# Optimization experiments

Hardware: AMD Instinct MI355X
Metric: run time of the kernel (lower is better)

Reference implementation:

```python
import jax, jax.numpy as jnp
import numpy as np

B, S, H, DH, W, G, M = 2, 4096, 12, 64, 256, 64, 256
D = H * DH  # 768
VOCAB = 50282
NEG = -1e9


def setup_inputs() -> dict:
    key = jax.random.key(0)
    ks = jax.random.split(key, 16)
    f = lambda k, shp, s=0.02: jax.random.normal(k, shp, jnp.float32) * s
    return {
        'input_ids': jax.random.randint(ks[0], (B, S), 0, VOCAB, jnp.int32),
        'attn_mask': jnp.ones((B, S), jnp.float32),
        'html_idx': jnp.sort(jax.random.randint(ks[1], (B, M), 0, S, jnp.int32), axis=-1),
        'embed': f(ks[2], (VOCAB, D), 1.0),
        'Wq': f(ks[3], (D, D)), 'bq': jnp.zeros((D,), jnp.float32),
        'Wk': f(ks[4], (D, D)), 'bk': jnp.zeros((D,), jnp.float32),
        'Wv': f(ks[5], (D, D)), 'bv': jnp.zeros((D,), jnp.float32),
        'Wo': f(ks[6], (D, D)), 'bo': jnp.zeros((D,), jnp.float32),
        'gamma': jnp.ones((D,), jnp.float32), 'beta': jnp.zeros((D,), jnp.float32),
        'Wp': f(ks[7], (D, D)), 'bp': jnp.zeros((D,), jnp.float32),
        'Wa': f(ks[8], (D, 3)), 'ba': jnp.zeros((3,), jnp.float32),
        'Ws': f(ks[9], (D, 2)), 'bs': jnp.zeros((2,), jnp.float32),
    }


def _band_shift(t, n_chunks):
    # t: [..., n_chunks+2, W, ...chunked along axis -3/-2]; gather 3 neighbor chunks
    return jnp.concatenate([t[..., i:i + n_chunks, :, :] for i in range(3)], axis=-2)


def longformer_hpt(input_ids, attn_mask, html_idx, embed, Wq, bq, Wk, bk, Wv, bv,
                   Wo, bo, gamma, beta, Wp, bp, Wa, ba, Ws, bs):
    x = embed[input_ids]  # [B,S,D]
    heads = lambda t: t.reshape(B, S, H, DH).transpose(0, 2, 1, 3)  # [B,H,S,DH]
    q, k, v = heads(x @ Wq + bq), heads(x @ Wk + bk), heads(x @ Wv + bv)
    scale = 1.0 / np.sqrt(DH).astype(np.float32)
    C = S // W  # chunks

    # --- sliding-window (banded) attention, one-sided window W ---
    kp = jnp.pad(k, ((0, 0), (0, 0), (W, W), (0, 0))).reshape(B, H, C + 2, W, DH)
    vp = jnp.pad(v, ((0, 0), (0, 0), (W, W), (0, 0))).reshape(B, H, C + 2, W, DH)
    k3 = _band_shift(kp, C)  # [B,H,C,3W,DH]
    v3 = _band_shift(vp, C)
    qc = q.reshape(B, H, C, W, DH)
    sb = jnp.einsum('bhcqd,bhckd->bhcqk', qc, k3) * scale  # [B,H,C,W,3W]

    ii = jnp.arange(W)[:, None]
    jj = jnp.arange(3 * W)[None, :]
    band_ok = jnp.abs(jj - W - ii) <= W  # [W,3W]
    keypos = jnp.arange(C)[:, None] * W - W + jnp.arange(3 * W)[None, :]  # [C,3W]
    kvalid = (keypos >= 0) & (keypos < S) & (keypos >= G)  # global keys handled separately
    mp = jnp.pad(attn_mask, ((0, 0), (W, W))).reshape(B, C + 2, W)
    m3 = jnp.concatenate([mp[:, i:i + C] for i in range(3)], axis=2)  # [B,C,3W]
    mask = band_ok[None, :, :] & kvalid[:, None, :] & (m3[:, :, None, :] > 0)[..., :, :].reshape(B, C, 1, 3 * W).astype(bool) if False else (band_ok[None, None, :, :] & kvalid[None, :, None, :] & (m3[:, :, None, :] > 0))  # [B,C,W,3W]
    sb = jnp.where(mask[:, None], sb, NEG).reshape(B, H, S, 3 * W)

    # --- all tokens also attend to the G global tokens ---
    kg, vg = k[:, :, :G], v[:, :, :G]
    sg = jnp.einsum('bhsd,bhgd->bhsg', q, kg) * scale
    sg = jnp.where(attn_mask[:, None, None, :G] > 0, sg, NEG)

    p = jax.nn.softmax(jnp.concatenate([sg, sb], -1), -1)  # [B,H,S,G+3W]
    pg, pb = p[..., :G], p[..., G:].reshape(B, H, C, W, 3 * W)
    out = (jnp.einsum('bhcqk,bhckd->bhcqd', pb, v3).reshape(B, H, S, DH)
           + jnp.einsum('bhsg,bhgd->bhsd', pg, vg))

    # --- global queries attend to everything ---
    sgl = jnp.einsum('bhgd,bhsd->bhgs', q[:, :, :G], k) * scale
    sgl = jnp.where(attn_mask[:, None, None, :] > 0, sgl, NEG)
    outg = jnp.einsum('bhgs,bhsd->bhgd', jax.nn.softmax(sgl, -1), v)
    out = jnp.concatenate([outg, out[:, :, G:]], axis=2)

    ctx = out.transpose(0, 2, 1, 3).reshape(B, S, D)
    h = x + ctx @ Wo + bo
    mu = h.mean(-1, keepdims=True)
    var = ((h - mu) ** 2).mean(-1, keepdims=True)
    hn = (h - mu) / jnp.sqrt(var + 1e-5) * gamma + beta  # last_hidden [B,S,D]

    # probes (ans_probe: Linear(768,3)+Sigmoid, span_probe: Linear(768,2)+Sigmoid)
    ans = jax.nn.sigmoid(hn @ Wa + ba)
    span = jax.nn.sigmoid(hn @ Ws + bs)

    # ReIndexer gather of HTML-element hidden states + ConditionCalculator
    hr = jnp.take_along_axis(hn, html_idx[:, :, None].astype(jnp.int32), axis=1)  # [B,M,D]
    t = jax.nn.relu(hr @ Wp + bp)
    cond = jax.nn.sigmoid(jnp.einsum('bqh,bch->bcq', hr, t))  # [B,M,M]
    return hn, ans, span, cond


def reference(input_ids, attn_mask, html_idx, embed, Wq, bq, Wk, bk, Wv, bv,
              Wo, bo, gamma, beta, Wp, bp, Wa, ba, Ws, bs):
    return longformer_hpt(input_ids, attn_mask, html_idx, embed, Wq, bq, Wk, bk,
                          Wv, bv, Wo, bo, gamma, beta, Wp, bp, Wa, ba, Ws, bs)
```

## Files before the change

### kernel.cpp

```cpp
#include <hip/hip_runtime.h>

typedef unsigned short u16;
typedef unsigned int   u32;
typedef __attribute__((ext_vector_type(8))) short s8v;
typedef __attribute__((ext_vector_type(8))) unsigned short us8;
typedef __attribute__((ext_vector_type(4))) float f4v;

constexpr int BC  = 2;
constexpr int SL  = 4096;
constexpr int NH  = 12;
constexpr int HD  = 64;
constexpr int DM  = 768;
constexpr int WIN = 256;
constexpr int GLB = 64;
constexpr int QN  = 2304;
constexpr int KCH = 16;
constexpr float FOLD = 0.125f * 1.44269504088896f;
constexpr float NEGS = -1.0e9f;

__device__ __forceinline__ float b2f(u16 b){ return __uint_as_float(((u32)b) << 16); }
__device__ __forceinline__ u16 f2b(float f){
  u32 u = __float_as_uint(f);
  return (u16)((u + 0x7fffu + ((u >> 16) & 1u)) >> 16);
}
__device__ __forceinline__ float wredsum(float v){
  #pragma unroll
  for (int o = 32; o > 0; o >>= 1) v += __shfl_xor(v, o, 64);
  return v;
}
__device__ __forceinline__ float sigf(float x){ return 1.f / (1.f + __expf(-x)); }

__global__ void transpose_pack(const float* __restrict__ src, u16* __restrict__ dst, int N){
  int e = blockIdx.x*256 + threadIdx.x;
  if (e >= N*768) return;
  int n = e / 768, k = e - n*768;
  dst[e] = f2b(src[(long)k*N + n]);
}

__global__ void pack_bias(const float* __restrict__ bq, const float* __restrict__ bk,
                          const float* __restrict__ bv, float* __restrict__ dst){
  int i = blockIdx.x*256 + threadIdx.x;
  if (i >= 2304) return;
  dst[i] = (i < 768) ? bq[i] : (i < 1536) ? bk[i-768] : bv[i-1536];
}

__global__ void embed_gather(const int* __restrict__ ids, const float* __restrict__ emb,
                             float* __restrict__ x, u16* __restrict__ xb){
  int e4 = blockIdx.x*256 + threadIdx.x;
  if (e4 >= 8192*192) return;
  int row = e4 / 192, d4 = e4 - row*192;
  int id = ids[row];
  float4 v = ((const float4*)(emb + (long)id*768))[d4];
  ((float4*)(x + (long)row*768))[d4] = v;
  u32 p0 = (u32)f2b(v.x) | ((u32)f2b(v.y) << 16);
  u32 p1 = (u32)f2b(v.z) | ((u32)f2b(v.w) << 16);
  ((u32*)(xb + (long)row*768))[d4*2]   = p0;
  ((u32*)(xb + (long)row*768))[d4*2+1] = p1;
}

__global__ void gather_hr(const int* __restrict__ hidx, const float* __restrict__ hn,
                          u16* __restrict__ hrb){
  int e = blockIdx.x*256 + threadIdx.x;
  if (e >= 512*768) return;
  int r = e / 768, d = e - r*768;
  int b = r >> 8;
  int idx = hidx[r];
  hrb[e] = f2b(hn[((long)(b*SL + idx))*768 + d]);
}

template<int MODE>
__global__ __launch_bounds__(256, 2)
void gemm_bt(const u16* __restrict__ A, const u16* __restrict__ Bt,
             const float* __restrict__ bias, const float* __restrict__ res,
             float* __restrict__ outF, u16* __restrict__ outB,
             int M, int N, int K, long sA, long sB, long sO)
{
  const int bz = blockIdx.z;
  A  += (long)bz * sA;
  Bt += (long)bz * sB;
  const int n0 = blockIdx.x * 128;
  const int m0 = blockIdx.y * 128;
  __shared__ u16 lsA[128*64];
  __shared__ u16 lsB[128*64];
  const int t = threadIdx.x;
  const int w = t >> 6, lane = t & 63;
  const int wr = w >> 1, wc = w & 1;
  const int fr = lane & 15, fq = lane >> 4;

  f4v acc[4][4];
  #pragma unroll
  for (int i=0;i<4;i++)
    #pragma unroll
    for (int j=0;j<4;j++) acc[i][j] = (f4v)0.f;

  for (int k0 = 0; k0 < K; k0 += 64){
    #pragma unroll
    for (int i=0;i<4;i++){
      int e = (w*4+i)*512 + lane*8;
      int row = e >> 6, col = e & 63;
      __builtin_amdgcn_global_load_lds(
        (const __attribute__((address_space(1))) void*)(A + (long)(m0+row)*K + (k0+col)),
        (__attribute__((address_space(3))) void*)(&lsA[(w*4+i)*512]), 16, 0, 0);
      __builtin_amdgcn_global_load_lds(
        (const __attribute__((address_space(1))) void*)(Bt + (long)(n0+row)*K + (k0+col)),
        (__attribute__((address_space(3))) void*)(&lsB[(w*4+i)*512]), 16, 0, 0);
    }
    __syncthreads();
    #pragma unroll
    for (int kk = 0; kk < 2; kk++){
      s8v af[4], bfv[4];
      #pragma unroll
      for (int mi=0;mi<4;mi++)
        af[mi] = *(const s8v*)&lsA[(wr*64 + mi*16 + fr)*64 + kk*32 + fq*8];
      #pragma unroll
      for (int ni=0;ni<4;ni++)
        bfv[ni] = *(const s8v*)&lsB[(wc*64 + ni*16 + fr)*64 + kk*32 + fq*8];
      #pragma unroll
      for (int mi=0;mi<4;mi++)
        #pragma unroll
        for (int ni=0;ni<4;ni++)
          acc[mi][ni] = __builtin_amdgcn_mfma_f32_16x16x32_bf16(af[mi], bfv[ni], acc[mi][ni], 0, 0, 0);
    }
    __syncthreads();
  }
  #pragma unroll
  for (int mi=0;mi<4;mi++){
    #pragma unroll
    for (int ni=0;ni<4;ni++){
      #pragma unroll
      for (int r=0;r<4;r++){
        int row = m0 + wr*64 + mi*16 + fq*4 + r;
        int col = n0 + wc*64 + ni*16 + fr;
        float v = acc[mi][ni][r];
        if constexpr (MODE == 0){
          v += bias[col];
          outB[(long)row*N + col] = f2b(v);
        } else if constexpr (MODE == 1){
          v += bias[col] + res[(long)row*N + col];
          outF[(long)row*N + col] = v;
        } else if constexpr (MODE == 2){
          v = fmaxf(v + bias[col], 0.f);
          outB[(long)row*N + col] = f2b(v);
        } else {
          (outF + bz*sO)[(long)row*N + col] = sigf(v);
        }
      }
    }
  }
}

__global__ __launch_bounds__(256, 2)
void attn_band_mfma(const u16* __restrict__ qkv, const float* __restrict__ mask, u16* __restrict__ ctx)
{
  const int q0 = blockIdx.x * 64;
  const int h = blockIdx.y, b = blockIdx.z;
  const int t = threadIdx.x;
  const int w = t >> 6, lane = t & 63;
  const int fq = lane >> 4, fr = lane & 15;

  __shared__ u16 lsK[64*64];
  __shared__ u16 lsVT[64*72];
  __shared__ u16 lsP[4][16*72];
  __shared__ float lsM[64];

  const long bq = (long)b*SL*QN;
  const u16* qrow = qkv + (bq + (long)(q0 + w*16 + fr)*QN) + h*HD;
  s8v aq[2];
  aq[0] = *(const s8v*)(qrow + fq*8);
  aq[1] = *(const s8v*)(qrow + 32 + fq*8);

  const u16* kq = qkv + bq + DM + h*HD;
  const u16* vq = qkv + bq + 2*DM + h*HD;
  const float* mrow = mask + b*SL;

  f4v out[4];
  #pragma unroll
  for (int n=0;n<4;n++) out[n] = (f4v)0.f;
  float m[4]  = {-3.0e38f,-3.0e38f,-3.0e38f,-3.0e38f};
  float l[4]  = {0.f,0.f,0.f,0.f};

  for (int ti = -1; ti < 9; ++ti){
    const int k0 = (ti < 0) ? 0 : (q0 - 256 + ti*64);
    if (ti >= 0 && (k0 < GLB || k0 >= SL)) continue;
    __syncthreads();
    if (t < 64) lsM[t] = mrow[k0 + t];
    #pragma unroll
    for (int j=0;j<2;j++){
      const int r = (w*2+j)*8 + (lane>>3);
      const int d = ((lane&7) ^ (lane>>3))*8;
      __builtin_amdgcn_global_load_lds(
        (const __attribute__((address_space(1))) void*)(kq + (long)(k0+r)*QN + d),
        (__attribute__((address_space(3))) void*)(&lsK[(w*2+j)*512]), 16, 0, 0);
    }
    #pragma unroll
    for (int j=0;j<2;j++){
      const int d0 = w*8 + j*32;
      us8 vv = *(const us8*)(vq + (long)(k0+lane)*QN + d0);
      #pragma unroll
      for (int jj=0;jj<8;jj++) lsVT[(d0+jj)*72 + lane] = (u16)vv[jj];
    }
    __syncthreads();

    f4v s[4];
    #pragma unroll
    for (int n=0;n<4;n++) s[n] = (f4v)0.f;
    #pragma unroll
    for (int kk=0;kk<2;kk++){
      #pragma unroll
      for (int n=0;n<4;n++){
        s8v bf = *(const s8v*)&lsK[(16*n+fr)*64 + (((kk*4+fq) ^ (fr&7))<<3)];
        s[n] = __builtin_amdgcn_mfma_f32_16x16x32_bf16(aq[kk], bf, s[n], 0,0,0);
      }
    }
    const bool isg = (ti < 0);
    #pragma unroll
    for (int n=0;n<4;n++){
      const int kcol = 16*n + fr;
      const float mk = lsM[kcol];
      #pragma unroll
      for (int r=0;r<4;r++){
        const int dd = k0 + kcol - (q0 + w*16 + fq*4 + r);
        const bool valid = (mk > 0.f) && (isg || (dd >= -WIN && dd <= WIN));
        s[n][r] = valid ? s[n][r]*FOLD : NEGS;
      }
    }
    float sf[4];
    #pragma unroll
    for (int r=0;r<4;r++){
      float rm = fmaxf(fmaxf(s[0][r], s[1][r]), fmaxf(s[2][r], s[3][r]));
      rm = fmaxf(rm, __shfl_xor(rm, 1, 64));
      rm = fmaxf(rm, __shfl_xor(rm, 2, 64));
      rm = fmaxf(rm, __shfl_xor(rm, 4, 64));
      rm = fmaxf(rm, __shfl_xor(rm, 8, 64));
      const float mn = fmaxf(m[r], rm);
      sf[r] = exp2f(m[r] - mn);
      m[r] = mn;
    }
    u16* lsPw = lsP[w];
    float rs[4] = {0.f,0.f,0.f,0.f};
    #pragma unroll
    for (int n=0;n<4;n++){
      #pragma unroll
      for (int r=0;r<4;r++){
        float p = exp2f(s[n][r] - m[r]);
        rs[r] += p;
        lsPw[(fq*4+r)*72 + 16*n + fr] = f2b(p);
        out[n][r] *= sf[r];
      }
    }
    #pragma unroll
    for (int r=0;r<4;r++){
      float rv = rs[r];
      rv += __shfl_xor(rv, 1, 64);
      rv += __shfl_xor(rv, 2, 64);
      rv += __shfl_xor(rv, 4, 64);
      rv += __shfl_xor(rv, 8, 64);
      l[r] = l[r]*sf[r] + rv;
    }
    s8v ap[2];
    ap[0] = *(const s8v*)&lsPw[fr*72 + fq*8];
    ap[1] = *(const s8v*)&lsPw[fr*72 + 32 + fq*8];
    #pragma unroll
    for (int kk=0;kk<2;kk++){
      #pragma unroll
      for (int n=0;n<4;n++){
        s8v bv = *(const s8v*)&lsVT[(16*n+fr)*72 + kk*32 + fq*8];
        out[n] = __builtin_amdgcn_mfma_f32_16x16x32_bf16(ap[kk], bv, out[n], 0,0,0);
      }
    }
  }
  #pragma unroll
  for (int r=0;r<4;r++) l[r] = 1.f/l[r];
  u16* cb = ctx + (((long)(b*SL) + q0 + w*16 + fq*4))*DM + h*HD + fr;
  #pragma unroll
  for (int n=0;n<4;n++)
    #pragma unroll
    for (int r=0;r<4;r++)
      cb[(long)r*DM + 16*n] = f2b(out[n][r]*l[r]);
}

__global__ __launch_bounds__(256, 2)
void attn_global_part(const u16* __restrict__ qkv, const float* __restrict__ mask,
                      float* __restrict__ pout, float* __restrict__ pml)
{
  const int ck = blockIdx.x;
  const int h = blockIdx.y, b = blockIdx.z;
  const int bh = b*NH + h;
  const int t = threadIdx.x;
  const int w = t >> 6, lane = t & 63;
  const int fq = lane >> 4, fr = lane & 15;

  __shared__ u16 lsK[64*64];
  __shared__ u16 lsVT[64*72];
  __shared__ u16 lsP[4][16*72];
  __shared__ float lsM[64];

  const long bq = (long)b*SL*QN;
  const u16* qrow = qkv + (bq + (long)(w*16 + fr)*QN) + h*HD;
  s8v aq[2];
  aq[0] = *(const s8v*)(qrow + fq*8);
  aq[1] = *(const s8v*)(qrow + 32 + fq*8);

  const u16* kq = qkv + bq + DM + h*HD;
  const u16* vq = qkv + bq + 2*DM + h*HD;
  const float* mrow = mask + b*SL;

  f4v out[4];
  #pragma unroll
  for (int n=0;n<4;n++) out[n] = (f4v)0.f;
  float m[4]  = {-3.0e38f,-3.0e38f,-3.0e38f,-3.0e38f};
  float l[4]  = {0.f,0.f,0.f,0.f};

  for (int ti = 0; ti < 4; ++ti){
    const int k0 = ck*256 + ti*64;
    __syncthreads();
    if (t < 64) lsM[t] = mrow[k0 + t];
    #pragma unroll
    for (int j=0;j<2;j++){
      const int r = (w*2+j)*8 + (lane>>3);
      const int d = ((lane&7) ^ (lane>>3))*8;
      __builtin_amdgcn_global_load_lds(
        (const __attribute__((address_space(1))) void*)(kq + (long)(k0+r)*QN + d),
        (__attribute__((address_space(3))) void*)(&lsK[(w*2+j)*512]), 16, 0, 0);
    }
    #pragma unroll
    for (int j=0;j<2;j++){
      const int d0 = w*8 + j*32;
      us8 vv = *(const us8*)(vq + (long)(k0+lane)*QN + d0);
      #pragma unroll
      for (int jj=0;jj<8;jj++) lsVT[(d0+jj)*72 + lane] = (u16)vv[jj];
    }
    __syncthreads();

    f4v s[4];
    #pragma unroll
    for (int n=0;n<4;n++) s[n] = (f4v)0.f;
    #pragma unroll
    for (int kk=0;kk<2;kk++){
      #pragma unroll
      for (int n=0;n<4;n++){
        s8v bf = *(const s8v*)&lsK[(16*n+fr)*64 + (((kk*4+fq) ^ (fr&7))<<3)];
        s[n] = __builtin_amdgcn_mfma_f32_16x16x32_bf16(aq[kk], bf, s[n], 0,0,0);
      }
    }
    #pragma unroll
    for (int n=0;n<4;n++){
      const float mk = lsM[16*n + fr];
      #pragma unroll
      for (int r=0;r<4;r++)
        s[n][r] = (mk > 0.f) ? s[n][r]*FOLD : NEGS;
    }
    float sf[4];
    #pragma unroll
    for (int r=0;r<4;r++){
      float rm = fmaxf(fmaxf(s[0][r], s[1][r]), fmaxf(s[2][r], s[3][r]));
      rm = fmaxf(rm, __shfl_xor(rm, 1, 64));
      rm = fmaxf(rm, __shfl_xor(rm, 2, 64));
      rm = fmaxf(rm, __shfl_xor(rm, 4, 64));
      rm = fmaxf(rm, __shfl_xor(rm, 8, 64));
      const float mn = fmaxf(m[r], rm);
      sf[r] = exp2f(m[r] - mn);
      m[r] = mn;
    }
    u16* lsPw = lsP[w];
    float rs[4] = {0.f,0.f,0.f,0.f};
    #pragma unroll
    for (int n=0;n<4;n++){
      #pragma unroll
      for (int r=0;r<4;r++){
        float p = exp2f(s[n][r] - m[r]);
        rs[r] += p;
        lsPw[(fq*4+r)*72 + 16*n + fr] = f2b(p);
        out[n][r] *= sf[r];
      }
    }
    #pragma unroll
    for (int r=0;r<4;r++){
      float rv = rs[r];
      rv += __shfl_xor(rv, 1, 64);
      rv += __shfl_xor(rv, 2, 64);
      rv += __shfl_xor(rv, 4, 64);
      rv += __shfl_xor(rv, 8, 64);
      l[r] = l[r]*sf[r] + rv;
    }
    s8v ap[2];
    ap[0] = *(const s8v*)&lsPw[fr*72 + fq*8];
    ap[1] = *(const s8v*)&lsPw[fr*72 + 32 + fq*8];
    #pragma unroll
    for (int kk=0;kk<2;kk++){
      #pragma unroll
      for (int n=0;n<4;n++){
        s8v bv = *(const s8v*)&lsVT[(16*n+fr)*72 + kk*32 + fq*8];
        out[n] = __builtin_amdgcn_mfma_f32_16x16x32_bf16(ap[kk], bv, out[n], 0,0,0);
      }
    }
  }
  float* pob = pout + ((long)(ck*BC*NH + bh))*64*64;
  #pragma unroll
  for (int n=0;n<4;n++)
    #pragma unroll
    for (int r=0;r<4;r++)
      pob[(w*16 + fq*4 + r)*64 + 16*n + fr] = out[n][r];
  if (fr == 0){
    float* pmb = pml + ((long)(ck*BC*NH + bh))*128;
    #pragma unroll
    for (int r=0;r<4;r++){
      pmb[(w*16 + fq*4 + r)*2 + 0] = m[r];
      pmb[(w*16 + fq*4 + r)*2 + 1] = l[r];
    }
  }
}

__global__ __launch_bounds__(256, 2)
void attn_global_combine(const float* __restrict__ pout, const float* __restrict__ pml,
                         u16* __restrict__ ctx)
{
  const int bh = blockIdx.x;
  const int b = bh / NH, h = bh % NH;
  const int t = threadIdx.x;
  __shared__ float wgt[KCH][64];
  __shared__ float rl[64];
  if (t < 64){
    float mc[KCH], lc[KCH];
    #pragma unroll
    for (int c = 0; c < KCH; c++){
      const float* pmb = pml + ((long)(c*BC*NH + bh))*128 + t*2;
      mc[c] = pmb[0]; lc[c] = pmb[1];
    }
    float M = mc[0];
    #pragma unroll
    for (int c = 1; c < KCH; c++) M = fmaxf(M, mc[c]);
    float L = 0.f;
    #pragma unroll
    for (int c = 0; c < KCH; c++){
      const float wv = exp2f(mc[c] - M);
      wgt[c][t] = wv;
      L += lc[c]*wv;
    }
    rl[t] = 1.f/L;
  }
  __syncthreads();
  const int row = t >> 2, dseg = t & 3;
  float acc[16];
  #pragma unroll
  for (int i=0;i<16;i++) acc[i] = 0.f;
  for (int c = 0; c < KCH; c++){
    const float wv = wgt[c][row];
    const float4* pb = (const float4*)(pout + ((long)(c*BC*NH + bh)*64 + row)*64 + dseg*16);
    #pragma unroll
    for (int i = 0; i < 4; i++){
      float4 v = pb[i];
      acc[i*4+0] += v.x*wv; acc[i*4+1] += v.y*wv;
      acc[i*4+2] += v.z*wv; acc[i*4+3] += v.w*wv;
    }
  }
  u16* cr = ctx + ((long)(b*SL + row))*DM + h*HD + dseg*16;
  const float r = rl[row];
  #pragma unroll
  for (int i = 0; i < 16; i += 2){
    u32 pk = (u32)f2b(acc[i]*r) | ((u32)f2b(acc[i+1]*r) << 16);
    *(u32*)(cr + i) = pk;
  }
}

__global__ __launch_bounds__(256, 2)
void ln_heads(const float* __restrict__ hbuf, const float* __restrict__ gamma, const float* __restrict__ beta,
              const float* __restrict__ Wa, const float* __restrict__ ba,
              const float* __restrict__ Wsp, const float* __restrict__ bsp,
              float* __restrict__ hn, float* __restrict__ ans, float* __restrict__ span)
{
  const int r = blockIdx.x;
  const int t = threadIdx.x, lane = t & 63, w = t >> 6;
  __shared__ float red[8];
  __shared__ float dred[4][5];
  const float* hrow = hbuf + (long)r*DM;
  float v0 = hrow[t], v1 = hrow[t+256], v2 = hrow[t+512];
  float sum = wredsum(v0 + v1 + v2);
  float sq  = wredsum(v0*v0 + v1*v1 + v2*v2);
  if (lane == 0){ red[w] = sum; red[4+w] = sq; }
  __syncthreads();
  const float mu  = (red[0]+red[1]+red[2]+red[3]) * (1.f/768.f);
  const float msq = (red[4]+red[5]+red[6]+red[7]) * (1.f/768.f);
  const float rstd = rsqrtf(msq - mu*mu + 1e-5f);
  float pa0=0,pa1=0,pa2=0,ps0=0,ps1=0;
  const long base = (long)r*DM;
  #pragma unroll
  for (int jj = 0; jj < 3; jj++){
    const int i = t + jj*256;
    const float hv = (jj==0) ? v0 : (jj==1) ? v1 : v2;
    const float y = (hv - mu)*rstd*gamma[i] + beta[i];
    hn[base + i] = y;
    pa0 += y*Wa[i*3+0]; pa1 += y*Wa[i*3+1]; pa2 += y*Wa[i*3+2];
    ps0 += y*Wsp[i*2+0]; ps1 += y*Wsp[i*2+1];
  }
  pa0 = wredsum(pa0); pa1 = wredsum(pa1); pa2 = wredsum(pa2);
  ps0 = wredsum(ps0); ps1 = wredsum(ps1);
  if (lane == 0){ dred[w][0]=pa0; dred[w][1]=pa1; dred[w][2]=pa2; dred[w][3]=ps0; dred[w][4]=ps1; }
  __syncthreads();
  if (t == 0){
    float A0 = dred[0][0]+dred[1][0]+dred[2][0]+dred[3][0];
    float A1 = dred[0][1]+dred[1][1]+dred[2][1]+dred[3][1];
    float A2 = dred[0][2]+dred[1][2]+dred[2][2]+dred[3][2];
    float S0 = dred[0][3]+dred[1][3]+dred[2][3]+dred[3][3];
    float S1 = dred[0][4]+dred[1][4]+dred[2][4]+dred[3][4];
    ans[(long)r*3+0]  = sigf(A0 + ba[0]);
    ans[(long)r*3+1]  = sigf(A1 + ba[1]);
    ans[(long)r*3+2]  = sigf(A2 + ba[2]);
    span[(long)r*2+0] = sigf(S0 + bsp[0]);
    span[(long)r*2+1] = sigf(S1 + bsp[1]);
  }
}

extern "C" void kernel_launch(void* const* d_in, const int* in_sizes, int n_in,
                              void* d_out, int out_size, void* d_ws, size_t ws_size,
                              hipStream_t stream)
{
  const int*   input_ids = (const int*)  d_in[0];
  const float* attn_mask = (const float*)d_in[1];
  const int*   html_idx  = (const int*)  d_in[2];
  const float* embed     = (const float*)d_in[3];
  const float* Wq = (const float*)d_in[4];  const float* bq = (const float*)d_in[5];
  const float* Wk = (const float*)d_in[6];  const float* bk = (const float*)d_in[7];
  const float* Wv = (const float*)d_in[8];  const float* bv = (const float*)d_in[9];
  const float* Wo = (const float*)d_in[10]; const float* bo = (const float*)d_in[11];
  const float* gamma = (const float*)d_in[12]; const float* beta = (const float*)d_in[13];
  const float* Wp = (const float*)d_in[14]; const float* bp = (const float*)d_in[15];
  const float* Wa = (const float*)d_in[16]; const float* ba = (const float*)d_in[17];
  const float* Wsp = (const float*)d_in[18]; const float* bsp = (const float*)d_in[19];

  char* ws = (char*)d_ws;
  size_t off = 0;
  auto take = [&](size_t bytes)->char*{
    char* p = ws + off; off += (bytes + 255) & ~(size_t)255; return p;
  };
  float* x_f    = (float*)take((size_t)8192*768*4);
  u16*   x_b    = (u16*)  take((size_t)8192*768*2);
  u16*   wt_qkv = (u16*)  take((size_t)2304*768*2);
  u16*   wt_o   = (u16*)  take((size_t)768*768*2);
  u16*   wt_p   = (u16*)  take((size_t)768*768*2);
  float* b_qkv  = (float*)take(2304*4);
  u16*   qkv_b  = (u16*)  take((size_t)8192*2304*2);
  u16*   ctx_b  = (u16*)  take((size_t)8192*768*2);
  float* h_f    = (float*)take((size_t)8192*768*4);
  u16*   hr_b   = (u16*)  take((size_t)512*768*2);
  u16*   t_b    = (u16*)  take((size_t)512*768*2);
  float* pout   = (float*)take((size_t)KCH*BC*NH*64*64*4);
  float* pml    = (float*)take((size_t)KCH*BC*NH*128*4);

  float* out_hn   = (float*)d_out;
  float* out_ans  = out_hn  + (size_t)8192*768;
  float* out_span = out_ans + (size_t)8192*3;
  float* out_cond = out_span + (size_t)8192*2;

  transpose_pack<<<2304, 256, 0, stream>>>(Wq, wt_qkv,             768);
  transpose_pack<<<2304, 256, 0, stream>>>(Wk, wt_qkv +   768*768, 768);
  transpose_pack<<<2304, 256, 0, stream>>>(Wv, wt_qkv + 2*768*768, 768);
  transpose_pack<<<2304, 256, 0, stream>>>(Wo, wt_o, 768);
  transpose_pack<<<2304, 256, 0, stream>>>(Wp, wt_p, 768);
  pack_bias<<<9, 256, 0, stream>>>(bq, bk, bv, b_qkv);
  embed_gather<<<6144, 256, 0, stream>>>(input_ids, embed, x_f, x_b);

  gemm_bt<0><<<dim3(18,64,1), 256, 0, stream>>>(x_b, wt_qkv, b_qkv, nullptr,
                                                nullptr, qkv_b, 8192, 2304, 768, 0,0,0);
  attn_band_mfma<<<dim3(64,12,2), 256, 0, stream>>>(qkv_b, attn_mask, ctx_b);
  attn_global_part<<<dim3(KCH,12,2), 256, 0, stream>>>(qkv_b, attn_mask, pout, pml);
  attn_global_combine<<<BC*NH, 256, 0, stream>>>(pout, pml, ctx_b);
  gemm_bt<1><<<dim3(6,64,1), 256, 0, stream>>>(ctx_b, wt_o, bo, x_f,
                                               h_f, nullptr, 8192, 768, 768, 0,0,0);
  ln_heads<<<8192, 256, 0, stream>>>(h_f, gamma, beta, Wa, ba, Wsp, bsp,
                                     out_hn, out_ans, out_span);
  gather_hr<<<1536, 256, 0, stream>>>(html_idx, out_hn, hr_b);
  gemm_bt<2><<<dim3(6,4,1), 256, 0, stream>>>(hr_b, wt_p, bp, nullptr,
                                              nullptr, t_b, 512, 768, 768, 0,0,0);
  gemm_bt<3><<<dim3(2,2,2), 256, 0, stream>>>(t_b, hr_b, nullptr, nullptr,
                                              out_cond, nullptr, 256, 256, 768,
                                              (long)256*768, (long)256*768, (long)256*256);
}
```

Measured before the change: 263.3 us.

## Double-buffer attention tiles, fuse weight packing, drop fp32 residual copy

Five per-matrix transpose launches and the bias pack are merged into one LDS-tiled transpose kernel with coalesced reads and writes. Both attention kernels now double-buffer K/V/mask tiles, prefetching the next tile while computing the current one. The band kernel computes its valid tile range up front instead of skipping tiles inside the loop, and occupancy hints rise to 3 blocks per SIMD. The fp32 embedding copy is removed and the residual is read from the bf16 copy, saving memory traffic but adding bf16 rounding to the residual path.

```diff
diff --git a/kernel.cpp b/kernel.cpp
--- a/kernel.cpp
+++ b/kernel.cpp
@@ -30,28 +30,49 @@
 }
 __device__ __forceinline__ float sigf(float x){ return 1.f / (1.f + __expf(-x)); }
 
-__global__ void transpose_pack(const float* __restrict__ src, u16* __restrict__ dst, int N){
-  int e = blockIdx.x*256 + threadIdx.x;
-  if (e >= N*768) return;
-  int n = e / 768, k = e - n*768;
-  dst[e] = f2b(src[(long)k*N + n]);
-}
-
-__global__ void pack_bias(const float* __restrict__ bq, const float* __restrict__ bk,
-                          const float* __restrict__ bv, float* __restrict__ dst){
-  int i = blockIdx.x*256 + threadIdx.x;
-  if (i >= 2304) return;
-  dst[i] = (i < 768) ? bq[i] : (i < 1536) ? bk[i-768] : bv[i-1536];
+__global__ void pack_w(const float* __restrict__ Wq, const float* __restrict__ Wk,
+                       const float* __restrict__ Wv, const float* __restrict__ Wo,
+                       const float* __restrict__ Wp,
+                       const float* __restrict__ bq, const float* __restrict__ bk,
+                       const float* __restrict__ bv,
+                       u16* __restrict__ wt_qkv, u16* __restrict__ wt_o,
+                       u16* __restrict__ wt_p, float* __restrict__ b_qkv)
+{
+  __shared__ float tile[64][65];
+  const int bid = blockIdx.x;
+  const int mi = bid / 144, rest = bid % 144;
+  const int kt = rest / 12, ntc = rest % 12;
+  const float* src = (mi==0)?Wq:(mi==1)?Wk:(mi==2)?Wv:(mi==3)?Wo:Wp;
+  u16* dst = (mi<3) ? (wt_qkv + (size_t)mi*768*768) : ((mi==3) ? wt_o : wt_p);
+  const int t = threadIdx.x;
+  const int k0 = kt*64, n0 = ntc*64;
+  #pragma unroll
+  for (int i=0;i<4;i++){
+    const int r = (t>>4) + i*16;
+    float4 v = ((const float4*)(src + (long)(k0+r)*768 + n0))[t&15];
+    tile[r][(t&15)*4+0] = v.x; tile[r][(t&15)*4+1] = v.y;
+    tile[r][(t&15)*4+2] = v.z; tile[r][(t&15)*4+3] = v.w;
+  }
+  __syncthreads();
+  const int n = t & 63, kc = (t>>6)*16;
+  u32* d32 = (u32*)(dst + (long)(n0+n)*768 + k0 + kc);
+  #pragma unroll
+  for (int i=0;i<8;i++){
+    d32[i] = (u32)f2b(tile[kc+2*i][n]) | ((u32)f2b(tile[kc+2*i+1][n]) << 16);
+  }
+  if (bid < 9){
+    const int i = bid*256 + t;
+    if (i < 2304) b_qkv[i] = (i < 768) ? bq[i] : (i < 1536) ? bk[i-768] : bv[i-1536];
+  }
 }
 
 __global__ void embed_gather(const int* __restrict__ ids, const float* __restrict__ emb,
-                             float* __restrict__ x, u16* __restrict__ xb){
+                             u16* __restrict__ xb){
   int e4 = blockIdx.x*256 + threadIdx.x;
   if (e4 >= 8192*192) return;
   int row = e4 / 192, d4 = e4 - row*192;
   int id = ids[row];
   float4 v = ((const float4*)(emb + (long)id*768))[d4];
-  ((float4*)(x + (long)row*768))[d4] = v;
   u32 p0 = (u32)f2b(v.x) | ((u32)f2b(v.y) << 16);
   u32 p1 = (u32)f2b(v.z) | ((u32)f2b(v.w) << 16);
   ((u32*)(xb + (long)row*768))[d4*2]   = p0;
@@ -71,7 +92,7 @@
 template<int MODE>
 __global__ __launch_bounds__(256, 2)
 void gemm_bt(const u16* __restrict__ A, const u16* __restrict__ Bt,
-             const float* __restrict__ bias, const float* __restrict__ res,
+             const float* __restrict__ bias, const u16* __restrict__ resB,
              float* __restrict__ outF, u16* __restrict__ outB,
              int M, int N, int K, long sA, long sB, long sO)
 {
@@ -136,7 +157,7 @@
           v += bias[col];
           outB[(long)row*N + col] = f2b(v);
         } else if constexpr (MODE == 1){
-          v += bias[col] + res[(long)row*N + col];
+          v += bias[col] + b2f(resB[(long)row*N + col]);
           outF[(long)row*N + col] = v;
         } else if constexpr (MODE == 2){
           v = fmaxf(v + bias[col], 0.f);
@@ -149,7 +170,7 @@
   }
 }
 
-__global__ __launch_bounds__(256, 2)
+__global__ __launch_bounds__(256, 3)
 void attn_band_mfma(const u16* __restrict__ qkv, const float* __restrict__ mask, u16* __restrict__ ctx)
 {
   const int q0 = blockIdx.x * 64;
@@ -158,10 +179,10 @@
   const int w = t >> 6, lane = t & 63;
   const int fq = lane >> 4, fr = lane & 15;
 
-  __shared__ u16 lsK[64*64];
-  __shared__ u16 lsVT[64*72];
+  __shared__ u16 lsK[2][64*64];
+  __shared__ u16 lsVT[2][64*72];
   __shared__ u16 lsP[4][16*72];
-  __shared__ float lsM[64];
+  __shared__ float lsM[2][64];
 
   const long bq = (long)b*SL*QN;
   const u16* qrow = qkv + (bq + (long)(q0 + w*16 + fr)*QN) + h*HD;
@@ -173,33 +194,45 @@
   const u16* vq = qkv + bq + 2*DM + h*HD;
   const float* mrow = mask + b*SL;
 
+  const int ti_lo = (q0 < 320) ? ((320 - q0) >> 6) : 0;
+  const int ti_hi_raw = (4352 - q0) >> 6;
+  const int ti_hi = ti_hi_raw < 9 ? ti_hi_raw : 9;
+  const int NTT = 1 + (ti_hi - ti_lo);
+  const int kb0 = q0 - 256 + ti_lo*64;
+
   f4v out[4];
   #pragma unroll
   for (int n=0;n<4;n++) out[n] = (f4v)0.f;
   float m[4]  = {-3.0e38f,-3.0e38f,-3.0e38f,-3.0e38f};
   float l[4]  = {0.f,0.f,0.f,0.f};
 
-  for (int ti = -1; ti < 9; ++ti){
-    const int k0 = (ti < 0) ? 0 : (q0 - 256 + ti*64);
-    if (ti >= 0 && (k0 < GLB || k0 >= SL)) continue;
-    __syncthreads();
-    if (t < 64) lsM[t] = mrow[k0 + t];
+  us8 vv0, vv1;
+  auto stage_issue = [&](int i, int buf){
+    const int k0 = (i == 0) ? 0 : kb0 + (i-1)*64;
+    if (t < 64) lsM[buf][t] = mrow[k0 + t];
     #pragma unroll
     for (int j=0;j<2;j++){
       const int r = (w*2+j)*8 + (lane>>3);
       const int d = ((lane&7) ^ (lane>>3))*8;
       __builtin_amdgcn_global_load_lds(
         (const __attribute__((address_space(1))) void*)(kq + (long)(k0+r)*QN + d),
-        (__attribute__((address_space(3))) void*)(&lsK[(w*2+j)*512]), 16, 0, 0);
-    }
-    #pragma unroll
-    for (int j=0;j<2;j++){
-      const int d0 = w*8 + j*32;
-      us8 vv = *(const us8*)(vq + (long)(k0+lane)*QN + d0);
-      #pragma unroll
-      for (int jj=0;jj<8;jj++) lsVT[(d0+jj)*72 + lane] = (u16)vv[jj];
-    }
+        (__attribute__((address_space(3))) void*)(&lsK[buf][(w*2+j)*512]), 16, 0, 0);
+    }
+    vv0 = *(const us8*)(vq + (long)(k0+lane)*QN + w*8);
+    vv1 = *(const us8*)(vq + (long)(k0+lane)*QN + w*8 + 32);
+  };
+
+  stage_issue(0, 0);
+  int cur = 0;
+  for (int i = 0; i < NTT; i++){
+    const int k0 = (i == 0) ? 0 : kb0 + (i-1)*64;
+    const int d0 = w*8;
+    #pragma unroll
+    for (int jj=0;jj<8;jj++) lsVT[cur][(d0+jj)*72 + lane] = (u16)vv0[jj];
+    #pragma unroll
+    for (int jj=0;jj<8;jj++) lsVT[cur][(d0+32+jj)*72 + lane] = (u16)vv1[jj];
     __syncthreads();
+    if (i+1 < NTT) stage_issue(i+1, cur^1);
 
     f4v s[4];
     #pragma unroll
@@ -208,15 +241,15 @@
     for (int kk=0;kk<2;kk++){
       #pragma unroll
       for (int n=0;n<4;n++){
-        s8v bf = *(const s8v*)&lsK[(16*n+fr)*64 + (((kk*4+fq) ^ (fr&7))<<3)];
+        s8v bf = *(const s8v*)&lsK[cur][(16*n+fr)*64 + (((kk*4+fq) ^ (fr&7))<<3)];
         s[n] = __builtin_amdgcn_mfma_f32_16x16x32_bf16(aq[kk], bf, s[n], 0,0,0);
       }
     }
-    const bool isg = (ti < 0);
+    const bool isg = (i == 0);
     #pragma unroll
     for (int n=0;n<4;n++){
       const int kcol = 16*n + fr;
-      const float mk = lsM[kcol];
+      const float mk = lsM[cur][kcol];
       #pragma unroll
       for (int r=0;r<4;r++){
         const int dd = k0 + kcol - (q0 + w*16 + fq*4 + r);
@@ -264,10 +297,11 @@
     for (int kk=0;kk<2;kk++){
       #pragma unroll
       for (int n=0;n<4;n++){
-        s8v bv = *(const s8v*)&lsVT[(16*n+fr)*72 + kk*32 + fq*8];
+        s8v bv = *(const s8v*)&lsVT[cur][(16*n+fr)*72 + kk*32 + fq*8];
         out[n] = __builtin_amdgcn_mfma_f32_16x16x32_bf16(ap[kk], bv, out[n], 0,0,0);
       }
     }
+    cur ^= 1;
   }
   #pragma unroll
   for (int r=0;r<4;r++) l[r] = 1.f/l[r];
@@ -279,7 +313,7 @@
       cb[(long)r*DM + 16*n] = f2b(out[n][r]*l[r]);
 }
 
-__global__ __launch_bounds__(256, 2)
+__global__ __launch_bounds__(256, 3)
 void attn_global_part(const u16* __restrict__ qkv, const float* __restrict__ mask,
                       float* __restrict__ pout, float* __restrict__ pml)
 {
@@ -290,10 +324,10 @@
   const int w = t >> 6, lane = t & 63;
   const int fq = lane >> 4, fr = lane & 15;
 
-  __shared__ u16 lsK[64*64];
-  __shared__ u16 lsVT[64*72];
+  __shared__ u16 lsK[2][64*64];
+  __shared__ u16 lsVT[2][64*72];
   __shared__ u16 lsP[4][16*72];
-  __shared__ float lsM[64];
+  __shared__ float lsM[2][64];
 
   const long bq = (long)b*SL*QN;
   const u16* qrow = qkv + (bq + (long)(w*16 + fr)*QN) + h*HD;
@@ -311,26 +345,32 @@
   float m[4]  = {-3.0e38f,-3.0e38f,-3.0e38f,-3.0e38f};
   float l[4]  = {0.f,0.f,0.f,0.f};
 
-  for (int ti = 0; ti < 4; ++ti){
-    const int k0 = ck*256 + ti*64;
-    __syncthreads();
-    if (t < 64) lsM[t] = mrow[k0 + t];
+  us8 vv0, vv1;
+  auto stage_issue = [&](int i, int buf){
+    const int k0 = ck*256 + i*64;
+    if (t < 64) lsM[buf][t] = mrow[k0 + t];
     #pragma unroll
     for (int j=0;j<2;j++){
       const int r = (w*2+j)*8 + (lane>>3);
       const int d = ((lane&7) ^ (lane>>3))*8;
       __builtin_amdgcn_global_load_lds(
         (const __attribute__((address_space(1))) void*)(kq + (long)(k0+r)*QN + d),
-        (__attribute__((address_space(3))) void*)(&lsK[(w*2+j)*512]), 16, 0, 0);
-    }
-    #pragma unroll
-    for (int j=0;j<2;j++){
-      const int d0 = w*8 + j*32;
-      us8 vv = *(const us8*)(vq + (long)(k0+lane)*QN + d0);
-      #pragma unroll
-      for (int jj=0;jj<8;jj++) lsVT[(d0+jj)*72 + lane] = (u16)vv[jj];
-    }
+        (__attribute__((address_space(3))) void*)(&lsK[buf][(w*2+j)*512]), 16, 0, 0);
+    }
+    vv0 = *(const us8*)(vq + (long)(k0+lane)*QN + w*8);
+    vv1 = *(const us8*)(vq + (long)(k0+lane)*QN + w*8 + 32);
+  };
+
+  stage_issue(0, 0);
+  int cur = 0;
+  for (int i = 0; i < 4; i++){
+    const int d0 = w*8;
+    #pragma unroll
+    for (int jj=0;jj<8;jj++) lsVT[cur][(d0+jj)*72 + lane] = (u16)vv0[jj];
+    #pragma unroll
+    for (int jj=0;jj<8;jj++) lsVT[cur][(d0+32+jj)*72 + lane] = (u16)vv1[jj];
     __syncthreads();
+    if (i+1 < 4) stage_issue(i+1, cur^1);
 
     f4v s[4];
     #pragma unroll
@@ -339,13 +379,13 @@
     for (int kk=0;kk<2;kk++){
       #pragma unroll
       for (int n=0;n<4;n++){
-        s8v bf = *(const s8v*)&lsK[(16*n+fr)*64 + (((kk*4+fq) ^ (fr&7))<<3)];
+        s8v bf = *(const s8v*)&lsK[cur][(16*n+fr)*64 + (((kk*4+fq) ^ (fr&7))<<3)];
         s[n] = __builtin_amdgcn_mfma_f32_16x16x32_bf16(aq[kk], bf, s[n], 0,0,0);
       }
     }
     #pragma unroll
     for (int n=0;n<4;n++){
-      const float mk = lsM[16*n + fr];
+      const float mk = lsM[cur][16*n + fr];
       #pragma unroll
       for (int r=0;r<4;r++)
         s[n][r] = (mk > 0.f) ? s[n][r]*FOLD : NEGS;
@@ -390,10 +430,11 @@
     for (int kk=0;kk<2;kk++){
       #pragma unroll
       for (int n=0;n<4;n++){
-        s8v bv = *(const s8v*)&lsVT[(16*n+fr)*72 + kk*32 + fq*8];
+        s8v bv = *(const s8v*)&lsVT[cur][(16*n+fr)*72 + kk*32 + fq*8];
         out[n] = __builtin_amdgcn_mfma_f32_16x16x32_bf16(ap[kk], bv, out[n], 0,0,0);
       }
     }
+    cur ^= 1;
   }
   float* pob = pout + ((long)(ck*BC*NH + bh))*64*64;
   #pragma unroll
@@ -533,7 +574,6 @@
   auto take = [&](size_t bytes)->char*{
     char* p = ws + off; off += (bytes + 255) & ~(size_t)255; return p;
   };
-  float* x_f    = (float*)take((size_t)8192*768*4);
   u16*   x_b    = (u16*)  take((size_t)8192*768*2);
   u16*   wt_qkv = (u16*)  take((size_t)2304*768*2);
   u16*   wt_o   = (u16*)  take((size_t)768*768*2);
@@ -552,20 +592,16 @@
   float* out_span = out_ans + (size_t)8192*3;
   float* out_cond = out_span + (size_t)8192*2;
 
-  transpose_pack<<<2304, 256, 0, stream>>>(Wq, wt_qkv,             768);
-  transpose_pack<<<2304, 256, 0, stream>>>(Wk, wt_qkv +   768*768, 768);
-  transpose_pack<<<2304, 256, 0, stream>>>(Wv, wt_qkv + 2*768*768, 768);
-  transpose_pack<<<2304, 256, 0, stream>>>(Wo, wt_o, 768);
-  transpose_pack<<<2304, 256, 0, stream>>>(Wp, wt_p, 768);
-  pack_bias<<<9, 256, 0, stream>>>(bq, bk, bv, b_qkv);
-  embed_gather<<<6144, 256, 0, stream>>>(input_ids, embed, x_f, x_b);
+  pack_w<<<720, 256, 0, stream>>>(Wq, Wk, Wv, Wo, Wp, bq, bk, bv,
+                                  wt_qkv, wt_o, wt_p, b_qkv);
+  embed_gather<<<6144, 256, 0, stream>>>(input_ids, embed, x_b);
 
   gemm_bt<0><<<dim3(18,64,1), 256, 0, stream>>>(x_b, wt_qkv, b_qkv, nullptr,
                                                 nullptr, qkv_b, 8192, 2304, 768, 0,0,0);
   attn_band_mfma<<<dim3(64,12,2), 256, 0, stream>>>(qkv_b, attn_mask, ctx_b);
   attn_global_part<<<dim3(KCH,12,2), 256, 0, stream>>>(qkv_b, attn_mask, pout, pml);
   attn_global_combine<<<BC*NH, 256, 0, stream>>>(pout, pml, ctx_b);
-  gemm_bt<1><<<dim3(6,64,1), 256, 0, stream>>>(ctx_b, wt_o, bo, x_f,
+  gemm_bt<1><<<dim3(6,64,1), 256, 0, stream>>>(ctx_b, wt_o, bo, x_b,
                                                h_f, nullptr, 8192, 768, 768, 0,0,0);
   ln_heads<<<8192, 256, 0, stream>>>(h_f, gamma, beta, Wa, ba, Wsp, bsp,
                                      out_hn, out_ans, out_span);
```

Measured after the change: 234.5 us. -10.9%, faster.
